# Kernel tuning notes

Measured on AMD Instinct MI355X. Metric: run time of the kernel, lower is better.

Reference implementation:

```python
import jax, jax.numpy as jnp
import numpy as np

NUM_HEADS = 8
EPS = 1e-6


def conv1x1(x, w, b):
    # x: [b,c,h,w], w: [out,in], b: [out]  (torch Conv2d 1x1 weight squeezed)
    return jnp.einsum('bchw,oc->bohw', x, w) + b[None, :, None, None]


def feature_map(x):
    return jax.nn.elu(x) + 1.0


def setup_inputs() -> dict:
    key = jax.random.key(0)
    ks = jax.random.split(key, 9)
    C = 512
    s = 1.0 / np.sqrt(C)
    x = jax.random.normal(ks[0], (8, C, 64, 64), dtype=jnp.float32)
    wq = jax.random.normal(ks[1], (C, C), dtype=jnp.float32) * s
    wk = jax.random.normal(ks[2], (C, C), dtype=jnp.float32) * s
    wv = jax.random.normal(ks[3], (C, C), dtype=jnp.float32) * s
    wo = jax.random.normal(ks[4], (C, C), dtype=jnp.float32) * s
    bq = jax.random.normal(ks[5], (C,), dtype=jnp.float32) * 0.01
    bk = jax.random.normal(ks[6], (C,), dtype=jnp.float32) * 0.01
    bv = jax.random.normal(ks[7], (C,), dtype=jnp.float32) * 0.01
    bo = jax.random.normal(ks[8], (C,), dtype=jnp.float32) * 0.01
    return {'x': x, 'wq': wq, 'bq': bq, 'wk': wk, 'bk': bk,
            'wv': wv, 'bv': bv, 'wo': wo, 'bo': bo}


def reference(x, wq, bq, wk, bk, wv, bv, wo, bo):
    b, c, h, w = x.shape
    nh = NUM_HEADS
    hd = c // nh
    L = h * w

    def to_heads(t):
        # [b,c,h,w] -> [b,nh,L,hd]
        return t.reshape(b, nh, hd, L).transpose(0, 1, 3, 2)

    Q = feature_map(to_heads(conv1x1(x, wq, bq)))
    K = feature_map(to_heads(conv1x1(x, wk, bk)))
    V = to_heads(conv1x1(x, wv, bv)) / L  # values / v_length

    KV = jnp.einsum('bhld,bhlv->bhdv', K, V)                 # [b,nh,hd,hd]
    Z = 1.0 / (jnp.einsum('bhld,bhd->bhl', Q, K.sum(axis=-2)) + EPS)
    out = jnp.einsum('bhld,bhdv,bhl->bhlv', Q, KV, Z) * L    # [b,nh,L,hd]

    out = out.transpose(0, 1, 3, 2).reshape(b, c, h, w)
    return conv1x1(out, wo, bo)
```

## Files before the change

kernel.cpp:

```cpp
#include <hip/hip_runtime.h>
#include <hip/hip_bf16.h>
#include <stdint.h>

#define BATCH 8
#define CCH   512
#define NHD   8
#define HD    64
#define LLEN  4096
#define M1    1536

typedef __bf16 bf16x8 __attribute__((ext_vector_type(8)));
typedef __bf16 bf16x4 __attribute__((ext_vector_type(4)));
typedef float  f32x4  __attribute__((ext_vector_type(4)));

__device__ __forceinline__ f32x4 mfma16(bf16x8 a, bf16x8 b, f32x4 c) {
  return __builtin_amdgcn_mfma_f32_16x16x32_bf16(a, b, c, 0, 0, 0);
}

__device__ __forceinline__ void gload_lds16(const void* g, void* l) {
  __builtin_amdgcn_global_load_lds(
      (const __attribute__((address_space(1))) uint32_t*)(uintptr_t)g,
      (__attribute__((address_space(3))) uint32_t*)(uintptr_t)l,
      16, 0, 0);
}

__global__ void pack_w(const float* __restrict__ wq, const float* __restrict__ wk,
                       const float* __restrict__ wv,
                       const float* __restrict__ bq, const float* __restrict__ bk,
                       const float* __restrict__ bv,
                       __bf16* __restrict__ wqkvb, float* __restrict__ biasq) {
  const int n = M1 * CCH + M1;
  for (int i = blockIdx.x * blockDim.x + threadIdx.x; i < n; i += gridDim.x * blockDim.x) {
    if (i < M1 * CCH) {
      int r = i >> 9, c = i & 511;
      float v = (r < 512) ? wq[r * 512 + c]
              : (r < 1024) ? wk[(r - 512) * 512 + c]
                           : wv[(r - 1024) * 512 + c];
      wqkvb[i] = (__bf16)v;
    } else {
      int j = i - M1 * CCH;
      biasq[j] = (j < 512) ? bq[j] : (j < 1024) ? bk[j - 512] : bv[j - 1024];
    }
  }
}

__global__ __launch_bounds__(256) void transpose_x(const float* __restrict__ x,
                                                   __bf16* __restrict__ xt) {
  __shared__ float tile[64][65];
  const int b = blockIdx.z, c0 = blockIdx.y * 64, l0 = blockIdx.x * 64;
  const int t = threadIdx.x;
  const int lq = (t & 15) * 4, cr = t >> 4;
  const float* xp = x + ((size_t)b * CCH + c0) * LLEN + l0;
#pragma unroll
  for (int q = 0; q < 4; ++q) {
    const int c = cr + q * 16;
    float4 v = *(const float4*)(xp + (size_t)c * LLEN + lq);
    tile[c][lq + 0] = v.x;
    tile[c][lq + 1] = v.y;
    tile[c][lq + 2] = v.z;
    tile[c][lq + 3] = v.w;
  }
  __syncthreads();
  __bf16* xo = xt + ((size_t)b * LLEN + l0) * CCH + c0;
  const int c4 = (t & 15) * 4, lr = t >> 4;
#pragma unroll
  for (int p = 0; p < 4; ++p) {
    const int l = lr + p * 16;
    bf16x4 o;
#pragma unroll
    for (int i = 0; i < 4; ++i) o[i] = (__bf16)tile[c4 + i][l];
    *(bf16x4*)(xo + (size_t)l * CCH + c4) = o;
  }
}

#define STAGE_A(tt)                                                           \
  {                                                                           \
    const int dbase = ((tt) & 3) * 16384;                                     \
    const int tK = (tt) * 32;                                                 \
    gload_lds16(Ag + srcOff + tK,         lds + dbase + tid * 8);             \
    gload_lds16(Ag + srcOff + tK + 65536, lds + dbase + 4096 + tid * 8);      \
  }
#define STAGE_B(tt)                                                           \
  {                                                                           \
    const int dbase = ((tt) & 3) * 16384 + 8192;                              \
    const int tK = (tt) * 32;                                                 \
    gload_lds16(Bg + srcOff + tK,         lds + dbase + tid * 8);             \
    gload_lds16(Bg + srcOff + tK + 65536, lds + dbase + 4096 + tid * 8);      \
  }

template <int EPI>
__global__ __launch_bounds__(512, 1) void gemm256(
    const __bf16* __restrict__ A, const __bf16* __restrict__ Bm,
    const float* __restrict__ bias,
    __bf16* __restrict__ qt, __bf16* __restrict__ kcm, __bf16* __restrict__ vcm,
    float* __restrict__ out) {
  __shared__ __attribute__((aligned(16))) __bf16 lds[4 * 16384];
  const int b  = blockIdx.z;
  const int n0 = blockIdx.x * 256;
  const int m0 = blockIdx.y * 256;
  const int tid = threadIdx.x;
  const int ll = tid & 63, w = tid >> 6;
  const int wr = w >> 2, wc = w & 3;
  const int lhi = ll >> 4, llo = ll & 15;

  const int slotE = ((lhi ^ ((llo >> 1) & 3)) << 3);
  int aOff[8], bOff[4];
#pragma unroll
  for (int m = 0; m < 8; ++m) aOff[m] = (wr * 128 + m * 16 + llo) * 32 + slotE;
#pragma unroll
  for (int n = 0; n < 4; ++n) bOff[n] = 8192 + (wc * 64 + n * 16 + llo) * 32 + slotE;

  const int sRow = tid >> 2;
  const int srcOff = sRow * CCH + ((((tid & 3) ^ ((sRow >> 1) & 3))) << 3);

  const __bf16* Ag = (EPI == 0 ? A + (size_t)m0 * CCH
                               : A + (size_t)b * CCH * CCH + (size_t)m0 * CCH);
  const __bf16* Bg = Bm + ((size_t)b * LLEN + n0) * CCH;

  f32x4 acc[8][4] = {};

  STAGE_A(0) STAGE_B(0) STAGE_A(1) STAGE_B(1) STAGE_A(2) STAGE_B(2)
  asm volatile("s_waitcnt vmcnt(8)" ::: "memory");
  __builtin_amdgcn_s_barrier();

  for (int t = 0; t < 16; ++t) {
    const int cb = (t & 3) * 16384;
    bf16x8 aq[8], bq[4];
#pragma unroll
    for (int m = 0; m < 8; ++m) aq[m] = *(const bf16x8*)(lds + cb + aOff[m]);
    bq[0] = *(const bf16x8*)(lds + cb + bOff[0]);
    bq[1] = *(const bf16x8*)(lds + cb + bOff[1]);
    if (t <= 12) STAGE_A(t + 3)
    __builtin_amdgcn_s_barrier();
    asm volatile("s_waitcnt lgkmcnt(0)" ::: "memory");
    __builtin_amdgcn_sched_barrier(0);
    __builtin_amdgcn_s_setprio(1);
#pragma unroll
    for (int m = 0; m < 8; ++m) {
      acc[m][0] = mfma16(aq[m], bq[0], acc[m][0]);
      acc[m][1] = mfma16(aq[m], bq[1], acc[m][1]);
    }
    __builtin_amdgcn_s_setprio(0);
    __builtin_amdgcn_s_barrier();
    bq[2] = *(const bf16x8*)(lds + cb + bOff[2]);
    bq[3] = *(const bf16x8*)(lds + cb + bOff[3]);
    if (t <= 12) STAGE_B(t + 3)
    if (t <= 12)      asm volatile("s_waitcnt vmcnt(8)" ::: "memory");
    else if (t == 13) asm volatile("s_waitcnt vmcnt(4)" ::: "memory");
    else if (t == 14) asm volatile("s_waitcnt vmcnt(0)" ::: "memory");
    __builtin_amdgcn_s_barrier();
    asm volatile("s_waitcnt lgkmcnt(0)" ::: "memory");
    __builtin_amdgcn_sched_barrier(0);
    __builtin_amdgcn_s_setprio(1);
#pragma unroll
    for (int m = 0; m < 8; ++m) {
      acc[m][2] = mfma16(aq[m], bq[2], acc[m][2]);
      acc[m][3] = mfma16(aq[m], bq[3], acc[m][3]);
    }
    __builtin_amdgcn_s_setprio(0);
    __builtin_amdgcn_s_barrier();
  }

#pragma unroll
  for (int i = 0; i < 8; ++i) {
    const int o0 = m0 + wr * 128 + i * 16 + lhi * 4;
#pragma unroll
    for (int j = 0; j < 4; ++j) {
      const int col = n0 + wc * 64 + j * 16 + llo;
      if (EPI == 0) {
        if (m0 < 512) {
          bf16x4 pk;
#pragma unroll
          for (int r = 0; r < 4; ++r) {
            float tv = acc[i][j][r] + bias[o0 + r];
            tv = tv > 0.f ? tv + 1.f : __expf(tv);
            pk[r] = (__bf16)tv;
          }
          *(bf16x4*)(qt + ((size_t)b * LLEN + col) * CCH + o0) = pk;
        } else if (m0 < 1024) {
#pragma unroll
          for (int r = 0; r < 4; ++r) {
            float tv = acc[i][j][r] + bias[o0 + r];
            tv = tv > 0.f ? tv + 1.f : __expf(tv);
            kcm[((size_t)b * CCH + (o0 - 512 + r)) * LLEN + col] = (__bf16)tv;
          }
        } else {
#pragma unroll
          for (int r = 0; r < 4; ++r)
            vcm[((size_t)b * CCH + (o0 - 1024 + r)) * LLEN + col] =
                (__bf16)(acc[i][j][r] + bias[o0 + r]);
        }
      } else {
#pragma unroll
        for (int r = 0; r < 4; ++r)
          out[((size_t)b * CCH + o0 + r) * LLEN + col] = acc[i][j][r] + bias[o0 + r];
      }
    }
  }
}

__global__ __launch_bounds__(256) void kv_part_k(const __bf16* __restrict__ kcm,
                                                 const __bf16* __restrict__ vcm,
                                                 float* __restrict__ part,
                                                 float* __restrict__ part_ks) {
  __shared__ float red[8192];
  __shared__ float ksred[4][64];
  const int lc = blockIdx.x, bh = blockIdx.y;
  const int b = bh >> 3, h = bh & 7;
  const int tid = threadIdx.x;
  const int w = tid >> 6, ll = tid & 63, lhi = ll >> 4, llo = ll & 15;
  const __bf16* Kp = kcm + ((size_t)b * CCH + h * 64) * LLEN;
  const __bf16* Vp = vcm + ((size_t)b * CCH + h * 64) * LLEN;
  f32x4 acc[4][4];
#pragma unroll
  for (int i = 0; i < 4; ++i)
#pragma unroll
    for (int j = 0; j < 4; ++j) acc[i][j] = (f32x4){0.f, 0.f, 0.f, 0.f};
  float ks[4] = {0.f, 0.f, 0.f, 0.f};
  const int base = lc * 512 + w * 128 + lhi * 8;
#pragma unroll
  for (int kt = 0; kt < 4; ++kt) {
    const int k0 = base + kt * 32;
    bf16x8 af[4], bfr[4];
#pragma unroll
    for (int i = 0; i < 4; ++i) af[i]  = *(const bf16x8*)(Kp + (size_t)(i * 16 + llo) * LLEN + k0);
#pragma unroll
    for (int i = 0; i < 4; ++i) bfr[i] = *(const bf16x8*)(Vp + (size_t)(i * 16 + llo) * LLEN + k0);
#pragma unroll
    for (int i = 0; i < 4; ++i)
#pragma unroll
      for (int r = 0; r < 8; ++r) ks[i] += (float)af[i][r];
#pragma unroll
    for (int i = 0; i < 4; ++i)
#pragma unroll
      for (int j = 0; j < 4; ++j) acc[i][j] = mfma16(af[i], bfr[j], acc[i][j]);
  }
#pragma unroll
  for (int i = 0; i < 4; ++i) {
    float s = ks[i];
    s += __shfl_xor(s, 16);
    s += __shfl_xor(s, 32);
    if (lhi == 0) ksred[w][i * 16 + llo] = s;
  }
  if (w >= 2) {
#pragma unroll
    for (int i = 0; i < 4; ++i)
#pragma unroll
      for (int j = 0; j < 4; ++j)
        *(f32x4*)(red + (((w - 2) * 16 + i * 4 + j) << 8) + ll * 4) = acc[i][j];
  }
  __syncthreads();
  if (w < 2) {
#pragma unroll
    for (int i = 0; i < 4; ++i)
#pragma unroll
      for (int j = 0; j < 4; ++j)
        acc[i][j] += *(const f32x4*)(red + ((w * 16 + i * 4 + j) << 8) + ll * 4);
  }
  float ksv = 0.f;
  if (w == 1) ksv = ksred[0][ll] + ksred[1][ll] + ksred[2][ll] + ksred[3][ll];
  __syncthreads();
  if (w == 1) {
#pragma unroll
    for (int i = 0; i < 4; ++i)
#pragma unroll
      for (int j = 0; j < 4; ++j)
        *(f32x4*)(red + ((i * 4 + j) << 8) + ll * 4) = acc[i][j];
    part_ks[((size_t)lc * 64 + bh) * 64 + ll] = ksv;
  }
  __syncthreads();
  if (w == 0) {
    float* op = part + ((size_t)lc * 64 + bh) * 4096;
#pragma unroll
    for (int i = 0; i < 4; ++i)
#pragma unroll
      for (int j = 0; j < 4; ++j) {
        acc[i][j] += *(const f32x4*)(red + ((i * 4 + j) << 8) + ll * 4);
#pragma unroll
        for (int r = 0; r < 4; ++r) {
          int d = i * 16 + lhi * 4 + r, v = j * 16 + llo;
          op[d * 64 + v] = acc[i][j][r];
        }
      }
  }
}

__global__ void kv_red_k(const float* __restrict__ part, float* __restrict__ kv) {
  const int i = blockIdx.x * blockDim.x + threadIdx.x;
  float s = 0.f;
#pragma unroll
  for (int lc = 0; lc < 8; ++lc) s += part[(size_t)lc * 262144 + i];
  kv[i] = s;
}

__global__ void ksum_red_k(const float* __restrict__ part_ks, float* __restrict__ ksum) {
  const int i = blockIdx.x * blockDim.x + threadIdx.x;
  float s = 0.f;
#pragma unroll
  for (int lc = 0; lc < 8; ++lc) s += part_ks[(size_t)lc * 4096 + i];
  ksum[i] = s;
}

__global__ __launch_bounds__(256) void fold_k(const float* __restrict__ wo,
                                              const float* __restrict__ kvb,
                                              __bf16* __restrict__ wokv) {
  const int h = blockIdx.x, b = blockIdx.y;
  const int tid = threadIdx.x;
  const int w = tid >> 6, ll = tid & 63, lhi = ll >> 4, llo = ll & 15;
  const float* kvp = kvb + (size_t)(b * 8 + h) * 4096;
  f32x4 acc[8][4] = {};
#pragma unroll
  for (int ks = 0; ks < 2; ++ks) {
    bf16x8 bfr[4];
#pragma unroll
    for (int n = 0; n < 4; ++n) {
      const float* p = kvp + (n * 16 + llo) * 64 + ks * 32 + lhi * 8;
      bf16x8 v;
#pragma unroll
      for (int e = 0; e < 8; ++e) v[e] = (__bf16)p[e];
      bfr[n] = v;
    }
#pragma unroll
    for (int m = 0; m < 8; ++m) {
      const float* p = wo + (size_t)(w * 128 + m * 16 + llo) * 512 + h * 64 + ks * 32 + lhi * 8;
      bf16x8 av;
#pragma unroll
      for (int e = 0; e < 8; ++e) av[e] = (__bf16)p[e];
#pragma unroll
      for (int n = 0; n < 4; ++n) acc[m][n] = mfma16(av, bfr[n], acc[m][n]);
    }
  }
#pragma unroll
  for (int m = 0; m < 8; ++m)
#pragma unroll
    for (int n = 0; n < 4; ++n)
#pragma unroll
      for (int r = 0; r < 4; ++r) {
        int o = w * 128 + m * 16 + lhi * 4 + r;
        int d = n * 16 + llo;
        wokv[((size_t)b * 512 + o) * 512 + h * 64 + d] = (__bf16)acc[m][n][r];
      }
}

__global__ __launch_bounds__(256) void zscale_k(__bf16* __restrict__ qt,
                                                const float* __restrict__ ksumf) {
  __shared__ float ks[512];
  const int b = blockIdx.y;
  const int l0 = blockIdx.x * 32;
  const int tid = threadIdx.x;
  ks[tid]       = ksumf[b * 512 + tid];
  ks[tid + 256] = ksumf[b * 512 + tid + 256];
  __syncthreads();
  const int r = tid >> 3, h = tid & 7;
  __bf16* qp = qt + ((size_t)b * LLEN + l0 + r) * CCH + h * 64;
  bf16x8 v[8];
  float dot = 0.f;
#pragma unroll
  for (int e = 0; e < 8; ++e) {
    v[e] = *(const bf16x8*)(qp + e * 8);
#pragma unroll
    for (int i = 0; i < 8; ++i) dot += (float)v[e][i] * ks[h * 64 + e * 8 + i];
  }
  const float z = 1.0f / (dot + 1e-6f);
#pragma unroll
  for (int e = 0; e < 8; ++e) {
    bf16x8 o;
#pragma unroll
    for (int i = 0; i < 8; ++i) o[i] = (__bf16)((float)v[e][i] * z);
    *(bf16x8*)(qp + e * 8) = o;
  }
}

extern "C" void kernel_launch(void* const* d_in, const int* in_sizes, int n_in,
                              void* d_out, int out_size, void* d_ws, size_t ws_size,
                              hipStream_t stream) {
  const float* x  = (const float*)d_in[0];
  const float* wq = (const float*)d_in[1];
  const float* bq = (const float*)d_in[2];
  const float* wk = (const float*)d_in[3];
  const float* bk = (const float*)d_in[4];
  const float* wv = (const float*)d_in[5];
  const float* bv = (const float*)d_in[6];
  const float* wo = (const float*)d_in[7];
  const float* bo = (const float*)d_in[8];
  float* out = (float*)d_out;

  char* p = (char*)d_ws;
  __bf16* xt    = (__bf16*)p; p += (size_t)BATCH * LLEN * CCH * 2;
  __bf16* qt    = (__bf16*)p; p += (size_t)BATCH * LLEN * CCH * 2;
  __bf16* kcm   = (__bf16*)p; p += (size_t)BATCH * CCH * LLEN * 2;
  __bf16* vcm   = (__bf16*)p; p += (size_t)BATCH * CCH * LLEN * 2;
  __bf16* wqkvb = (__bf16*)p; p += (size_t)M1 * CCH * 2;
  float*  biasq = (float*)p;  p += (size_t)M1 * 4;
  float*  ksumf = (float*)p;  p += (size_t)BATCH * CCH * 4;
  float*  part  = (float*)p;  p += (size_t)8 * 64 * HD * HD * 4;
  float*  kvb   = (float*)p;  p += (size_t)64 * HD * HD * 4;
  float*  pks   = (float*)p;  p += (size_t)8 * 64 * 64 * 4;
  __bf16* wokv  = (__bf16*)p; p += (size_t)BATCH * CCH * CCH * 2;

  pack_w<<<1024, 256, 0, stream>>>(wq, wk, wv, bq, bk, bv, wqkvb, biasq);
  transpose_x<<<dim3(64, 8, BATCH), 256, 0, stream>>>(x, xt);
  gemm256<0><<<dim3(16, 6, BATCH), 512, 0, stream>>>(wqkvb, xt, biasq, qt, kcm, vcm, nullptr);
  kv_part_k<<<dim3(8, 64), 256, 0, stream>>>(kcm, vcm, part, pks);
  kv_red_k<<<1024, 256, 0, stream>>>(part, kvb);
  ksum_red_k<<<16, 256, 0, stream>>>(pks, ksumf);
  fold_k<<<dim3(8, 8), 256, 0, stream>>>(wo, kvb, wokv);
  zscale_k<<<dim3(128, BATCH), 256, 0, stream>>>(qt, ksumf);
  gemm256<1><<<dim3(16, 2, BATCH), 512, 0, stream>>>(wokv, qt, bo, nullptr, nullptr, vcm, out);
}
```

Baseline: 187.7 us.

## Switch GEMMs to 128x128 tiles, fuse KV reductions into fold, widen transpose stores

Replaces the 256x256 four-stage GEMM (one 512-thread block per CU) with a 128x128 double-buffered GEMM using 256 threads and up to four blocks per CU. The aim is more blocks and better latency hiding through occupancy rather than a hand-scheduled pipeline. The KV and k-sum reduction kernels are merged into the fold kernel, dropping two launches and the kvb buffer. The transpose now writes 16-byte vectors instead of 8-byte ones. The cost is less data reuse per block and the loss of the explicit barrier, priority and waitcnt scheduling.

```diff
diff --git a/kernel.cpp b/kernel.cpp
--- a/kernel.cpp
+++ b/kernel.cpp
@@ -62,108 +62,84 @@
   }
   __syncthreads();
   __bf16* xo = xt + ((size_t)b * LLEN + l0) * CCH + c0;
-  const int c4 = (t & 15) * 4, lr = t >> 4;
-#pragma unroll
-  for (int p = 0; p < 4; ++p) {
-    const int l = lr + p * 16;
-    bf16x4 o;
-#pragma unroll
-    for (int i = 0; i < 4; ++i) o[i] = (__bf16)tile[c4 + i][l];
-    *(bf16x4*)(xo + (size_t)l * CCH + c4) = o;
-  }
-}
-
-#define STAGE_A(tt)                                                           \
-  {                                                                           \
-    const int dbase = ((tt) & 3) * 16384;                                     \
-    const int tK = (tt) * 32;                                                 \
-    gload_lds16(Ag + srcOff + tK,         lds + dbase + tid * 8);             \
-    gload_lds16(Ag + srcOff + tK + 65536, lds + dbase + 4096 + tid * 8);      \
-  }
-#define STAGE_B(tt)                                                           \
-  {                                                                           \
-    const int dbase = ((tt) & 3) * 16384 + 8192;                              \
-    const int tK = (tt) * 32;                                                 \
-    gload_lds16(Bg + srcOff + tK,         lds + dbase + tid * 8);             \
-    gload_lds16(Bg + srcOff + tK + 65536, lds + dbase + 4096 + tid * 8);      \
+  const int c8 = (t & 7) * 8, lr = t >> 3;
+#pragma unroll
+  for (int p = 0; p < 2; ++p) {
+    const int l = lr + p * 32;
+    bf16x8 o;
+#pragma unroll
+    for (int i = 0; i < 8; ++i) o[i] = (__bf16)tile[c8 + i][l];
+    *(bf16x8*)(xo + (size_t)l * CCH + c8) = o;
+  }
+}
+
+#define STG128(tt, buf)                                                      \
+  {                                                                          \
+    const __bf16* As_ = Ag + (tt) * 32;                                      \
+    const __bf16* Bs_ = Bg + (tt) * 32;                                      \
+    __bf16* dA = lds + (buf) * 8192;                                         \
+    __bf16* dB = dA + 4096;                                                  \
+    gload_lds16(As_ + srcOff1, dA + tid * 8);                                \
+    gload_lds16(As_ + srcOff2, dA + tid * 8 + 2048);                         \
+    gload_lds16(Bs_ + srcOff1, dB + tid * 8);                                \
+    gload_lds16(Bs_ + srcOff2, dB + tid * 8 + 2048);                         \
   }
 
 template <int EPI>
-__global__ __launch_bounds__(512, 1) void gemm256(
+__global__ __launch_bounds__(256, 4) void gemm128(
     const __bf16* __restrict__ A, const __bf16* __restrict__ Bm,
     const float* __restrict__ bias,
     __bf16* __restrict__ qt, __bf16* __restrict__ kcm, __bf16* __restrict__ vcm,
     float* __restrict__ out) {
-  __shared__ __attribute__((aligned(16))) __bf16 lds[4 * 16384];
+  __shared__ __attribute__((aligned(16))) __bf16 lds[2 * 8192];
   const int b  = blockIdx.z;
-  const int n0 = blockIdx.x * 256;
-  const int m0 = blockIdx.y * 256;
+  const int n0 = blockIdx.x * 128;
+  const int m0 = blockIdx.y * 128;
   const int tid = threadIdx.x;
   const int ll = tid & 63, w = tid >> 6;
-  const int wr = w >> 2, wc = w & 3;
+  const int wr = w >> 1, wc = w & 1;
   const int lhi = ll >> 4, llo = ll & 15;
 
   const int slotE = ((lhi ^ ((llo >> 1) & 3)) << 3);
-  int aOff[8], bOff[4];
-#pragma unroll
-  for (int m = 0; m < 8; ++m) aOff[m] = (wr * 128 + m * 16 + llo) * 32 + slotE;
-#pragma unroll
-  for (int n = 0; n < 4; ++n) bOff[n] = 8192 + (wc * 64 + n * 16 + llo) * 32 + slotE;
-
-  const int sRow = tid >> 2;
-  const int srcOff = sRow * CCH + ((((tid & 3) ^ ((sRow >> 1) & 3))) << 3);
+  int aOff[4], bOff[4];
+#pragma unroll
+  for (int m = 0; m < 4; ++m) aOff[m] = (wr * 64 + m * 16 + llo) * 32 + slotE;
+#pragma unroll
+  for (int n = 0; n < 4; ++n) bOff[n] = 4096 + (wc * 64 + n * 16 + llo) * 32 + slotE;
+
+  const int s1 = tid, s2 = tid + 256;
+  const int r1 = s1 >> 2, r2s = s2 >> 2;
+  const int srcOff1 = r1 * CCH + (((s1 & 3) ^ ((r1 >> 1) & 3)) << 3);
+  const int srcOff2 = r2s * CCH + (((s2 & 3) ^ ((r2s >> 1) & 3)) << 3);
 
   const __bf16* Ag = (EPI == 0 ? A + (size_t)m0 * CCH
                                : A + (size_t)b * CCH * CCH + (size_t)m0 * CCH);
   const __bf16* Bg = Bm + ((size_t)b * LLEN + n0) * CCH;
 
-  f32x4 acc[8][4] = {};
-
-  STAGE_A(0) STAGE_B(0) STAGE_A(1) STAGE_B(1) STAGE_A(2) STAGE_B(2)
-  asm volatile("s_waitcnt vmcnt(8)" ::: "memory");
-  __builtin_amdgcn_s_barrier();
+  f32x4 acc[4][4] = {};
+
+  STG128(0, 0)
+  __syncthreads();
 
   for (int t = 0; t < 16; ++t) {
-    const int cb = (t & 3) * 16384;
-    bf16x8 aq[8], bq[4];
-#pragma unroll
-    for (int m = 0; m < 8; ++m) aq[m] = *(const bf16x8*)(lds + cb + aOff[m]);
-    bq[0] = *(const bf16x8*)(lds + cb + bOff[0]);
-    bq[1] = *(const bf16x8*)(lds + cb + bOff[1]);
-    if (t <= 12) STAGE_A(t + 3)
-    __builtin_amdgcn_s_barrier();
-    asm volatile("s_waitcnt lgkmcnt(0)" ::: "memory");
-    __builtin_amdgcn_sched_barrier(0);
-    __builtin_amdgcn_s_setprio(1);
-#pragma unroll
-    for (int m = 0; m < 8; ++m) {
-      acc[m][0] = mfma16(aq[m], bq[0], acc[m][0]);
-      acc[m][1] = mfma16(aq[m], bq[1], acc[m][1]);
-    }
-    __builtin_amdgcn_s_setprio(0);
-    __builtin_amdgcn_s_barrier();
-    bq[2] = *(const bf16x8*)(lds + cb + bOff[2]);
-    bq[3] = *(const bf16x8*)(lds + cb + bOff[3]);
-    if (t <= 12) STAGE_B(t + 3)
-    if (t <= 12)      asm volatile("s_waitcnt vmcnt(8)" ::: "memory");
-    else if (t == 13) asm volatile("s_waitcnt vmcnt(4)" ::: "memory");
-    else if (t == 14) asm volatile("s_waitcnt vmcnt(0)" ::: "memory");
-    __builtin_amdgcn_s_barrier();
-    asm volatile("s_waitcnt lgkmcnt(0)" ::: "memory");
-    __builtin_amdgcn_sched_barrier(0);
-    __builtin_amdgcn_s_setprio(1);
-#pragma unroll
-    for (int m = 0; m < 8; ++m) {
-      acc[m][2] = mfma16(aq[m], bq[2], acc[m][2]);
-      acc[m][3] = mfma16(aq[m], bq[3], acc[m][3]);
-    }
-    __builtin_amdgcn_s_setprio(0);
-    __builtin_amdgcn_s_barrier();
-  }
-
-#pragma unroll
-  for (int i = 0; i < 8; ++i) {
-    const int o0 = m0 + wr * 128 + i * 16 + lhi * 4;
+    const int buf = t & 1;
+    if (t < 15) STG128(t + 1, buf ^ 1)
+    bf16x8 af[4], bfr[4];
+    const __bf16* base = lds + buf * 8192;
+#pragma unroll
+    for (int m = 0; m < 4; ++m) af[m] = *(const bf16x8*)(base + aOff[m]);
+#pragma unroll
+    for (int n = 0; n < 4; ++n) bfr[n] = *(const bf16x8*)(base + bOff[n]);
+#pragma unroll
+    for (int m = 0; m < 4; ++m)
+#pragma unroll
+      for (int n = 0; n < 4; ++n) acc[m][n] = mfma16(af[m], bfr[n], acc[m][n]);
+    __syncthreads();
+  }
+
+#pragma unroll
+  for (int i = 0; i < 4; ++i) {
+    const int o0 = m0 + wr * 64 + i * 16 + lhi * 4;
 #pragma unroll
     for (int j = 0; j < 4; ++j) {
       const int col = n0 + wc * 64 + j * 16 + llo;
@@ -285,36 +261,37 @@
   }
 }
 
-__global__ void kv_red_k(const float* __restrict__ part, float* __restrict__ kv) {
-  const int i = blockIdx.x * blockDim.x + threadIdx.x;
-  float s = 0.f;
-#pragma unroll
-  for (int lc = 0; lc < 8; ++lc) s += part[(size_t)lc * 262144 + i];
-  kv[i] = s;
-}
-
-__global__ void ksum_red_k(const float* __restrict__ part_ks, float* __restrict__ ksum) {
-  const int i = blockIdx.x * blockDim.x + threadIdx.x;
-  float s = 0.f;
-#pragma unroll
-  for (int lc = 0; lc < 8; ++lc) s += part_ks[(size_t)lc * 4096 + i];
-  ksum[i] = s;
-}
-
-__global__ __launch_bounds__(256) void fold_k(const float* __restrict__ wo,
-                                              const float* __restrict__ kvb,
-                                              __bf16* __restrict__ wokv) {
+__global__ __launch_bounds__(256) void kvfold_k(const float* __restrict__ part,
+                                                const float* __restrict__ pks,
+                                                const float* __restrict__ wo,
+                                                __bf16* __restrict__ wokv,
+                                                float* __restrict__ ksumf) {
+  __shared__ float kvred[64 * 68];
   const int h = blockIdx.x, b = blockIdx.y;
+  const int bh = b * 8 + h;
   const int tid = threadIdx.x;
+  for (int i = tid; i < 4096; i += 256) {
+    float s = 0.f;
+#pragma unroll
+    for (int lc = 0; lc < 8; ++lc) s += part[(size_t)lc * 262144 + (size_t)bh * 4096 + i];
+    kvred[(i >> 6) * 68 + (i & 63)] = s;
+  }
+  if (tid < 64) {
+    float s = 0.f;
+#pragma unroll
+    for (int lc = 0; lc < 8; ++lc) s += pks[(size_t)lc * 4096 + bh * 64 + tid];
+    ksumf[b * 512 + h * 64 + tid] = s;
+  }
+  __syncthreads();
+
   const int w = tid >> 6, ll = tid & 63, lhi = ll >> 4, llo = ll & 15;
-  const float* kvp = kvb + (size_t)(b * 8 + h) * 4096;
   f32x4 acc[8][4] = {};
 #pragma unroll
   for (int ks = 0; ks < 2; ++ks) {
     bf16x8 bfr[4];
 #pragma unroll
     for (int n = 0; n < 4; ++n) {
-      const float* p = kvp + (n * 16 + llo) * 64 + ks * 32 + lhi * 8;
+      const float* p = kvred + (n * 16 + llo) * 68 + ks * 32 + lhi * 8;
       bf16x8 v;
 #pragma unroll
       for (int e = 0; e < 8; ++e) v[e] = (__bf16)p[e];
@@ -394,17 +371,15 @@
   float*  biasq = (float*)p;  p += (size_t)M1 * 4;
   float*  ksumf = (float*)p;  p += (size_t)BATCH * CCH * 4;
   float*  part  = (float*)p;  p += (size_t)8 * 64 * HD * HD * 4;
-  float*  kvb   = (float*)p;  p += (size_t)64 * HD * HD * 4;
   float*  pks   = (float*)p;  p += (size_t)8 * 64 * 64 * 4;
   __bf16* wokv  = (__bf16*)p; p += (size_t)BATCH * CCH * CCH * 2;
 
   pack_w<<<1024, 256, 0, stream>>>(wq, wk, wv, bq, bk, bv, wqkvb, biasq);
   transpose_x<<<dim3(64, 8, BATCH), 256, 0, stream>>>(x, xt);
-  gemm256<0><<<dim3(16, 6, BATCH), 512, 0, stream>>>(wqkvb, xt, biasq, qt, kcm, vcm, nullptr);
+  gemm128<0><<<dim3(32, 12, BATCH), 256, 0, stream>>>(wqkvb, xt, biasq, qt, kcm, vcm, nullptr);
   kv_part_k<<<dim3(8, 64), 256, 0, stream>>>(kcm, vcm, part, pks);
-  kv_red_k<<<1024, 256, 0, stream>>>(part, kvb);
-  ksum_red_k<<<16, 256, 0, stream>>>(pks, ksumf);
-  fold_k<<<dim3(8, 8), 256, 0, stream>>>(wo, kvb, wokv);
+  kvfold_k<<<dim3(8, BATCH), 256, 0, stream>>>(part, pks, wo, wokv, ksumf);
   zscale_k<<<dim3(128, BATCH), 256, 0, stream>>>(qt, ksumf);
-  gemm256<1><<<dim3(16, 2, BATCH), 512, 0, stream>>>(wokv, qt, bo, nullptr, nullptr, vcm, out);
-}
+  gemm128<1><<<dim3(32, 4, BATCH), 256, 0, stream>>>(wokv, qt, bo, nullptr, nullptr,
+                                                     nullptr, out);
+}
```

New measurement: 182.7 us. -2.7%, faster.
